# Optimization experiments

Measured on AMD Instinct MI355X. Metric: run time of the kernel, lower is better.

Reference implementation:

```python
import jax, jax.numpy as jnp
import numpy as np

N, F_IN, H1, H2, E = 100000, 256, 128, 64, 1600000


def _glorot(key, shape):
    lim = np.sqrt(6.0 / (shape[0] + shape[1]))
    return jax.random.uniform(key, shape, jnp.float32, -lim, lim)


def setup_inputs() -> dict:
    key = jax.random.key(0)
    ks = jax.random.split(key, 8)
    x = jax.random.normal(ks[0], (N, F_IN), jnp.float32)
    edge_index = jax.random.randint(ks[1], (2, E), 0, N, jnp.int64)
    return {
        "x": x,
        "w1": _glorot(ks[2], (F_IN, H1)),
        "b1": jnp.zeros((H1,), jnp.float32),
        "w2": _glorot(ks[3], (H1, H2)),
        "b2": jnp.zeros((H2,), jnp.float32),
        "w3": _glorot(ks[4], (H1, H2)),
        "b3": jnp.zeros((H2,), jnp.float32),
        "edge_index": edge_index,
    }


def _gcn_conv(x, w, b, src, dst, dinv_sqrt):
    # GCNConv: transform first, then symmetric-normalized aggregation with self-loops.
    h = x @ w                                   # [N, out]
    coef = dinv_sqrt[src] * dinv_sqrt[dst]      # [E]
    agg = jnp.zeros_like(h).at[dst].add(h[src] * coef[:, None])
    # self-loop contribution: coefficient deg^-1 per node
    agg = agg + h * (dinv_sqrt * dinv_sqrt)[:, None]
    return agg + b


def reference(x, w1, b1, w2, b2, w3, b3, edge_index):
    src, dst = edge_index[0], edge_index[1]
    n = x.shape[0]
    # degree including self-loop (edge weights all 1)
    deg = jnp.ones((n,), x.dtype).at[dst].add(1.0)
    dinv_sqrt = jax.lax.rsqrt(deg)
    hidden = jax.nn.relu(_gcn_conv(x, w1, b1, src, dst, dinv_sqrt))
    mu = _gcn_conv(hidden, w2, b2, src, dst, dinv_sqrt)
    logvar = _gcn_conv(hidden, w3, b3, src, dst, dinv_sqrt)
    return (mu, logvar)
```

## Files before the change

kernel.cpp:

```cpp
#include <hip/hip_runtime.h>


#define TPB 256
#define GSHIFT 9
#define GSIZE 512
#define PART_M 8192

typedef __attribute__((ext_vector_type(8))) short short8;
typedef __attribute__((ext_vector_type(4))) short short4v;
typedef __attribute__((ext_vector_type(4))) float floatx4;
typedef __attribute__((ext_vector_type(4))) unsigned int uint4v;

__device__ __forceinline__ void split2(float v, short& hi, short& lo) {
    unsigned u = __float_as_uint(v);
    float hf = __uint_as_float(u & 0xFFFF0000u);
    float lf = v - hf;
    hi = (short)(u >> 16);
    lo = (short)(__float_as_uint(lf) >> 16);
}

__device__ __forceinline__ short bf16_rtn(float v) {
    unsigned u = __float_as_uint(v);
    u += 0x7FFF + ((u >> 16) & 1);
    return (short)(u >> 16);
}

__device__ __forceinline__ void addrow(float* a, uint4v v) {
    a[0] += __uint_as_float(v[0] << 16); a[1] += __uint_as_float(v[0] & 0xFFFF0000u);
    a[2] += __uint_as_float(v[1] << 16); a[3] += __uint_as_float(v[1] & 0xFFFF0000u);
    a[4] += __uint_as_float(v[2] << 16); a[5] += __uint_as_float(v[2] & 0xFFFF0000u);
    a[6] += __uint_as_float(v[3] << 16); a[7] += __uint_as_float(v[3] & 0xFFFF0000u);
}

__device__ __forceinline__ void gather_accum(float* acc, const int* __restrict__ csr,
                                             int start, int deg, const uint4v* hp,
                                             int lane) {
    int j = 0;
    for (; j + 3 < deg; j += 4) {
        int s0 = csr[start + j], s1 = csr[start + j + 1];
        int s2 = csr[start + j + 2], s3 = csr[start + j + 3];
        uint4v v0 = hp[(size_t)s0 * 16 + lane];
        uint4v v1 = hp[(size_t)s1 * 16 + lane];
        uint4v v2 = hp[(size_t)s2 * 16 + lane];
        uint4v v3 = hp[(size_t)s3 * 16 + lane];
        addrow(acc, v0);
        addrow(acc, v1);
        addrow(acc, v2);
        addrow(acc, v3);
    }
    if (j + 1 < deg) {
        int s0 = csr[start + j], s1 = csr[start + j + 1];
        uint4v v0 = hp[(size_t)s0 * 16 + lane];
        uint4v v1 = hp[(size_t)s1 * 16 + lane];
        addrow(acc, v0);
        addrow(acc, v1);
        j += 2;
    }
    if (j < deg) addrow(acc, hp[(size_t)csr[start + j] * 16 + lane]);
}

__device__ __forceinline__ void gload_lds16(const void* g, void* l) {
    __builtin_amdgcn_global_load_lds(
        (const __attribute__((address_space(1))) unsigned int*)g,
        (__attribute__((address_space(3))) unsigned int*)l, 16, 0, 0);
}

__global__ __launch_bounds__(TPB) void prep_all(const float* __restrict__ w1,
                                                const float* __restrict__ w2,
                                                const float* __restrict__ b2,
                                                const float* __restrict__ w3,
                                                const float* __restrict__ b3,
                                                short* __restrict__ w1t_h,
                                                short* __restrict__ w1t_l,
                                                short* __restrict__ wct_h,
                                                short* __restrict__ wct_l,
                                                float* __restrict__ bcat,
                                                int* __restrict__ cursor) {
    int b = blockIdx.x, t0 = threadIdx.x;
    if (b < 128) {
        int t = b * TPB + t0;
        int k = t & 255, n = t >> 8;
        float v = w1[(size_t)k * 128 + n];
        short h, l;
        split2(v, h, l);
        w1t_h[t] = h;
        w1t_l[t] = l;
    } else if (b < 192) {
        int t = (b - 128) * TPB + t0;
        int k = t & 127, n = t >> 7;
        float v = (n < 64) ? w2[(size_t)k * 64 + n] : w3[(size_t)k * 64 + (n - 64)];
        short h, l;
        split2(v, h, l);
        wct_h[t] = h;
        wct_l[t] = l;
        if (t < 64) { bcat[t] = b2[t]; bcat[64 + t] = b3[t]; }
    } else {
        for (int i = t0; i < 513; i += TPB) cursor[i] = 0;
    }
}

__global__ __launch_bounds__(TPB) void group_count(const int* __restrict__ dst,
                                                   int* __restrict__ cursor, int E) {
    int* ghist = cursor;
    int* done  = cursor + 512;
    int* goff  = cursor + 513;
    __shared__ int h[256];
    __shared__ int lastFlag;
    int t = threadIdx.x;
    h[t] = 0;
    __syncthreads();
    const int4* d4 = (const int4*)dst;
    int E4 = E >> 2;
    int stride = gridDim.x * TPB;
    for (int k = blockIdx.x * TPB + t; k < E4; k += stride) {
        int4 v = d4[k];
        atomicAdd(&h[v.x >> GSHIFT], 1);
        atomicAdd(&h[v.y >> GSHIFT], 1);
        atomicAdd(&h[v.z >> GSHIFT], 1);
        atomicAdd(&h[v.w >> GSHIFT], 1);
    }
    for (int k = (E4 << 2) + blockIdx.x * TPB + t; k < E; k += stride)
        atomicAdd(&h[dst[k] >> GSHIFT], 1);
    __syncthreads();
    if (h[t]) atomicAdd(&ghist[t], h[t]);
    __threadfence();
    __syncthreads();
    if (t == 0) lastFlag = (atomicAdd(done, 1) == (int)gridDim.x - 1);
    __syncthreads();
    if (!lastFlag) return;
    int v = atomicAdd(&ghist[t], 0);
    h[t] = v;
    __syncthreads();
#pragma unroll
    for (int off = 1; off < 256; off <<= 1) {
        int x = (t >= off) ? h[t - off] : 0;
        __syncthreads();
        h[t] += x;
        __syncthreads();
    }
    goff[t] = h[t] - v;
    if (t == 255) goff[256] = h[255];
}

__global__ __launch_bounds__(256) void partition_kernel(const int* __restrict__ src,
                                                        const int* __restrict__ dst,
                                                        const int* __restrict__ goff,
                                                        int* __restrict__ gcur,
                                                        int* __restrict__ staged, int E) {
    __shared__ int sorted[PART_M];
    __shared__ int sc[256];
    __shared__ int lstart[257];
    __shared__ int cur[256];
    __shared__ int gb[256];
    int t = threadIdx.x;
    int base = blockIdx.x * PART_M;
    int mloc = min(PART_M, E - base);
    int m4 = mloc >> 2;

    sc[t] = 0;
    cur[t] = 0;
    __syncthreads();
    const int4* d4 = (const int4*)(dst + base);
    const int4* s4 = (const int4*)(src + base);
    for (int k = t; k < m4; k += 256) {
        int4 v = d4[k];
        atomicAdd(&sc[v.x >> GSHIFT], 1);
        atomicAdd(&sc[v.y >> GSHIFT], 1);
        atomicAdd(&sc[v.z >> GSHIFT], 1);
        atomicAdd(&sc[v.w >> GSHIFT], 1);
    }
    for (int k = (m4 << 2) + t; k < mloc; k += 256)
        atomicAdd(&sc[dst[base + k] >> GSHIFT], 1);
    __syncthreads();
    int v = sc[t];
    __syncthreads();
    sc[t] = v;
    __syncthreads();
#pragma unroll
    for (int off = 1; off < 256; off <<= 1) {
        int x = (t >= off) ? sc[t - off] : 0;
        __syncthreads();
        sc[t] += x;
        __syncthreads();
    }
    lstart[t] = sc[t] - v;
    if (t == 255) lstart[256] = sc[255];
    gb[t] = goff[t] + atomicAdd(&gcur[t], v);
    __syncthreads();
    for (int k = t; k < m4; k += 256) {
        int4 dv = d4[k];
        int4 sv = s4[k];
        int b0 = dv.x >> GSHIFT;
        sorted[lstart[b0] + atomicAdd(&cur[b0], 1)] = (sv.x << GSHIFT) | (dv.x & (GSIZE - 1));
        int b1 = dv.y >> GSHIFT;
        sorted[lstart[b1] + atomicAdd(&cur[b1], 1)] = (sv.y << GSHIFT) | (dv.y & (GSIZE - 1));
        int b2 = dv.z >> GSHIFT;
        sorted[lstart[b2] + atomicAdd(&cur[b2], 1)] = (sv.z << GSHIFT) | (dv.z & (GSIZE - 1));
        int b3 = dv.w >> GSHIFT;
        sorted[lstart[b3] + atomicAdd(&cur[b3], 1)] = (sv.w << GSHIFT) | (dv.w & (GSIZE - 1));
    }
    for (int k = (m4 << 2) + t; k < mloc; k += 256) {
        int d = dst[base + k];
        int s = src[base + k];
        int b = d >> GSHIFT;
        sorted[lstart[b] + atomicAdd(&cur[b], 1)] = (s << GSHIFT) | (d & (GSIZE - 1));
    }
    __syncthreads();
    for (int e = t; e < mloc; e += 256) {
        int lo = 0, hi = 256;
        while (hi - lo > 1) {
            int mid = (lo + hi) >> 1;
            if (lstart[mid] <= e) lo = mid; else hi = mid;
        }
        staged[gb[lo] + (e - lstart[lo])] = sorted[e];
    }
}

__global__ __launch_bounds__(512) void build_csr(const int* __restrict__ staged,
                                                 const int* __restrict__ goff,
                                                 int* __restrict__ cnt,
                                                 float* __restrict__ dinv,
                                                 int* __restrict__ rowptr,
                                                 int* __restrict__ csr, int N) {
    __shared__ int hist[512];
    __shared__ int sc[512];
    __shared__ int lrow[512];
    __shared__ int cur[512];
    int t = threadIdx.x;
    int g = blockIdx.x;
    int s0 = goff[g], s1 = goff[g + 1];
    hist[t] = 0;
    cur[t] = 0;
    __syncthreads();
    for (int k = s0 + t; k < s1; k += 512)
        atomicAdd(&hist[staged[k] & (GSIZE - 1)], 1);
    __syncthreads();
    int v = hist[t];
    sc[t] = v;
    __syncthreads();
#pragma unroll
    for (int off = 1; off < 512; off <<= 1) {
        int x = (t >= off) ? sc[t - off] : 0;
        __syncthreads();
        sc[t] += x;
        __syncthreads();
    }
    int rp = s0 + sc[t] - v;
    lrow[t] = rp;
    int node = (g << GSHIFT) + t;
    if (node < N) {
        rowptr[node] = rp;
        cnt[node] = v;
        dinv[node] = rsqrtf(1.0f + (float)v);
    }
    __syncthreads();
    for (int k = s0 + t; k < s1; k += 512) {
        int p = staged[k];
        int dl = p & (GSIZE - 1);
        int pos = lrow[dl] + atomicAdd(&cur[dl], 1);
        csr[pos] = p >> GSHIFT;
    }
}

__global__ __launch_bounds__(TPB) void gemm_mfma_f32in(const float* __restrict__ A,
                                                       const short* __restrict__ Bth,
                                                       const short* __restrict__ Btl,
                                                       const float* __restrict__ rs,
                                                       short* __restrict__ Cb, int M, int K) {
    __shared__ float Af[2][64 * 32];
    __shared__ short Bh[2][128 * 32];
    __shared__ short Bl[2][128 * 32];
    int t = threadIdx.x;
    int wave = t >> 6, lane = t & 63, quad = lane >> 4, l16 = lane & 15;
    int bm0 = blockIdx.x * 64;

    floatx4 acc[8];
#pragma unroll
    for (int nt = 0; nt < 8; ++nt) acc[nt] = (floatx4){0.f, 0.f, 0.f, 0.f};

    auto stage = [&](int pb, int k0) {
#pragma unroll
        for (int i = 0; i < 2; ++i) {
            int g = i * 256 + t;
            int row = g >> 3, col = g & 7;
            int gr = bm0 + row;
            if (gr >= M) gr = M - 1;
            int scol = col ^ (row & 7);
            gload_lds16(A + (size_t)gr * K + k0 + scol * 4,
                        &Af[pb][(i * 256 + wave * 64) * 4]);
        }
#pragma unroll
        for (int i = 0; i < 2; ++i) {
            int g = i * 256 + t;
            int row = g >> 2, col = g & 3;
            int scol = col ^ ((row >> 1) & 3);
            size_t off = (size_t)row * K + k0 + scol * 8;
            int lb = (i * 256 + wave * 64) * 8;
            gload_lds16(Bth + off, &Bh[pb][lb]);
            gload_lds16(Btl + off, &Bl[pb][lb]);
        }
    };

    int nk = K >> 5;
    stage(0, 0);
    __syncthreads();
    int am = wave * 16 + l16;
    int ac0 = ((quad * 2 + 0) ^ (am & 7)) * 4;
    int ac1 = ((quad * 2 + 1) ^ (am & 7)) * 4;
    int bc = (quad ^ ((l16 >> 1) & 3)) * 8;
    for (int ks = 0; ks < nk; ++ks) {
        int pb = ks & 1;
        if (ks + 1 < nk) stage(pb ^ 1, (ks + 1) << 5);
        float4 fa0 = *(const float4*)&Af[pb][am * 32 + ac0];
        float4 fa1 = *(const float4*)&Af[pb][am * 32 + ac1];
        short8 a_h, a_l;
        {
            short h, l;
            split2(fa0.x, h, l); a_h[0] = h; a_l[0] = l;
            split2(fa0.y, h, l); a_h[1] = h; a_l[1] = l;
            split2(fa0.z, h, l); a_h[2] = h; a_l[2] = l;
            split2(fa0.w, h, l); a_h[3] = h; a_l[3] = l;
            split2(fa1.x, h, l); a_h[4] = h; a_l[4] = l;
            split2(fa1.y, h, l); a_h[5] = h; a_l[5] = l;
            split2(fa1.z, h, l); a_h[6] = h; a_l[6] = l;
            split2(fa1.w, h, l); a_h[7] = h; a_l[7] = l;
        }
#pragma unroll
        for (int nt = 0; nt < 8; ++nt) {
            int bn = nt * 16 + l16;
            short8 b_h = *(const short8*)&Bh[pb][bn * 32 + bc];
            short8 b_l = *(const short8*)&Bl[pb][bn * 32 + bc];
            acc[nt] = __builtin_amdgcn_mfma_f32_16x16x32_bf16(a_l, b_h, acc[nt], 0, 0, 0);
            acc[nt] = __builtin_amdgcn_mfma_f32_16x16x32_bf16(a_h, b_l, acc[nt], 0, 0, 0);
            acc[nt] = __builtin_amdgcn_mfma_f32_16x16x32_bf16(a_h, b_h, acc[nt], 0, 0, 0);
        }
        __syncthreads();
    }
#pragma unroll
    for (int reg = 0; reg < 4; ++reg) {
        int gr = bm0 + wave * 16 + quad * 4 + reg;
        if (gr < M) {
            float s = rs[gr];
            short* cp = Cb + (size_t)gr * 128;
#pragma unroll
            for (int nt = 0; nt < 8; ++nt) cp[nt * 16 + l16] = bf16_rtn(acc[nt][reg] * s);
        }
    }
}

__global__ __launch_bounds__(TPB) void gemm_mfma_bfin(const short* __restrict__ AH,
                                                      const short* __restrict__ AL,
                                                      const short* __restrict__ Bth,
                                                      const short* __restrict__ Btl,
                                                      const float* __restrict__ rs,
                                                      short* __restrict__ Cb, int M, int K) {
    __shared__ short Ah[2][64 * 32], Al[2][64 * 32];
    __shared__ short Bh[2][128 * 32], Bl[2][128 * 32];
    int t = threadIdx.x;
    int wave = t >> 6, lane = t & 63, quad = lane >> 4, l16 = lane & 15;
    int bm0 = blockIdx.x * 64;

    floatx4 acc[8];
#pragma unroll
    for (int nt = 0; nt < 8; ++nt) acc[nt] = (floatx4){0.f, 0.f, 0.f, 0.f};

    auto stage = [&](int pb, int k0) {
        {
            int row = t >> 2, col = t & 3;
            int gr = bm0 + row;
            if (gr >= M) gr = M - 1;
            int scol = col ^ ((row >> 1) & 3);
            size_t off = (size_t)gr * K + k0 + scol * 8;
            int lb = (wave * 64) * 8;
            gload_lds16(AH + off, &Ah[pb][lb]);
            gload_lds16(AL + off, &Al[pb][lb]);
        }
#pragma unroll
        for (int i = 0; i < 2; ++i) {
            int g = i * 256 + t;
            int row = g >> 2, col = g & 3;
            int scol = col ^ ((row >> 1) & 3);
            size_t off = (size_t)row * K + k0 + scol * 8;
            int lb = (i * 256 + wave * 64) * 8;
            gload_lds16(Bth + off, &Bh[pb][lb]);
            gload_lds16(Btl + off, &Bl[pb][lb]);
        }
    };

    int nk = K >> 5;
    stage(0, 0);
    __syncthreads();
    int am = wave * 16 + l16;
    int ac = (quad ^ ((am >> 1) & 3)) * 8;
    int bc = (quad ^ ((l16 >> 1) & 3)) * 8;
    for (int ks = 0; ks < nk; ++ks) {
        int pb = ks & 1;
        if (ks + 1 < nk) stage(pb ^ 1, (ks + 1) << 5);
        short8 a_h = *(const short8*)&Ah[pb][am * 32 + ac];
        short8 a_l = *(const short8*)&Al[pb][am * 32 + ac];
#pragma unroll
        for (int nt = 0; nt < 8; ++nt) {
            int bn = nt * 16 + l16;
            short8 b_h = *(const short8*)&Bh[pb][bn * 32 + bc];
            short8 b_l = *(const short8*)&Bl[pb][bn * 32 + bc];
            acc[nt] = __builtin_amdgcn_mfma_f32_16x16x32_bf16(a_l, b_h, acc[nt], 0, 0, 0);
            acc[nt] = __builtin_amdgcn_mfma_f32_16x16x32_bf16(a_h, b_l, acc[nt], 0, 0, 0);
            acc[nt] = __builtin_amdgcn_mfma_f32_16x16x32_bf16(a_h, b_h, acc[nt], 0, 0, 0);
        }
        __syncthreads();
    }
#pragma unroll
    for (int reg = 0; reg < 4; ++reg) {
        int gr = bm0 + wave * 16 + quad * 4 + reg;
        if (gr < M) {
            float s = rs[gr];
            short* cp = Cb + (size_t)gr * 128;
#pragma unroll
            for (int nt = 0; nt < 8; ++nt) cp[nt * 16 + l16] = bf16_rtn(acc[nt][reg] * s);
        }
    }
}

__global__ __launch_bounds__(TPB) void gather_hidden(const int* __restrict__ csr,
                                                     const int* __restrict__ rowptr,
                                                     const int* __restrict__ cnt,
                                                     const float* __restrict__ dinv,
                                                     const short* __restrict__ hs,
                                                     const float* __restrict__ b1,
                                                     short* __restrict__ hidH,
                                                     short* __restrict__ hidL, int N) {
    size_t t = (size_t)blockIdx.x * TPB + threadIdx.x;
    int nid = (int)(t >> 4);
    int lane = threadIdx.x & 15;
    if (nid >= N) return;
    int start = rowptr[nid];
    int deg = cnt[nid];
    const uint4v* hp = (const uint4v*)hs;
    float acc[8] = {0, 0, 0, 0, 0, 0, 0, 0};
    addrow(acc, __builtin_nontemporal_load(&hp[(size_t)nid * 16 + lane]));
    gather_accum(acc, csr, start, deg, hp, lane);
    float di = dinv[nid];
    float4 b0 = ((const float4*)b1)[lane * 2];
    float4 b1v = ((const float4*)b1)[lane * 2 + 1];
    float bb[8] = {b0.x, b0.y, b0.z, b0.w, b1v.x, b1v.y, b1v.z, b1v.w};
    unsigned hiw[8];
    short low[8];
#pragma unroll
    for (int i = 0; i < 8; ++i) {
        float h = fmaxf(fmaf(di, acc[i], bb[i]), 0.f);
        unsigned u = __float_as_uint(h);
        hiw[i] = u >> 16;
        float hf = __uint_as_float(u & 0xFFFF0000u);
        low[i] = bf16_rtn(h - hf);
    }
    uint4v ph, pl;
    ph[0] = hiw[0] | (hiw[1] << 16);
    ph[1] = hiw[2] | (hiw[3] << 16);
    ph[2] = hiw[4] | (hiw[5] << 16);
    ph[3] = hiw[6] | (hiw[7] << 16);
    pl[0] = (unsigned short)low[0] | ((unsigned)(unsigned short)low[1] << 16);
    pl[1] = (unsigned short)low[2] | ((unsigned)(unsigned short)low[3] << 16);
    pl[2] = (unsigned short)low[4] | ((unsigned)(unsigned short)low[5] << 16);
    pl[3] = (unsigned short)low[6] | ((unsigned)(unsigned short)low[7] << 16);
    __builtin_nontemporal_store(ph, &((uint4v*)hidH)[(size_t)nid * 16 + lane]);
    __builtin_nontemporal_store(pl, &((uint4v*)hidL)[(size_t)nid * 16 + lane]);
}

__global__ __launch_bounds__(TPB) void gather_out(const int* __restrict__ csr,
                                                  const int* __restrict__ rowptr,
                                                  const int* __restrict__ cnt,
                                                  const float* __restrict__ dinv,
                                                  const short* __restrict__ hs,
                                                  const float* __restrict__ bcat,
                                                  float* __restrict__ out, int N) {
    size_t t = (size_t)blockIdx.x * TPB + threadIdx.x;
    int nid = (int)(t >> 4);
    int lane = threadIdx.x & 15;
    if (nid >= N) return;
    int start = rowptr[nid];
    int deg = cnt[nid];
    const uint4v* hp = (const uint4v*)hs;
    float acc[8] = {0, 0, 0, 0, 0, 0, 0, 0};
    addrow(acc, __builtin_nontemporal_load(&hp[(size_t)nid * 16 + lane]));
    gather_accum(acc, csr, start, deg, hp, lane);
    float di = dinv[nid];
    float4 b0 = ((const float4*)bcat)[lane * 2];
    float4 b1v = ((const float4*)bcat)[lane * 2 + 1];
    floatx4 r0, r1;
    r0[0] = fmaf(di, acc[0], b0.x);
    r0[1] = fmaf(di, acc[1], b0.y);
    r0[2] = fmaf(di, acc[2], b0.z);
    r0[3] = fmaf(di, acc[3], b0.w);
    r1[0] = fmaf(di, acc[4], b1v.x);
    r1[1] = fmaf(di, acc[5], b1v.y);
    r1[2] = fmaf(di, acc[6], b1v.z);
    r1[3] = fmaf(di, acc[7], b1v.w);
    int f = lane * 8;
    float* dp = (f < 64) ? (out + (size_t)nid * 64 + f)
                         : (out + (size_t)N * 64 + (size_t)nid * 64 + (f - 64));
    __builtin_nontemporal_store(r0, (floatx4*)dp);
    __builtin_nontemporal_store(r1, (floatx4*)(dp + 4));
}

extern "C" void kernel_launch(void* const* d_in, const int* in_sizes, int n_in,
                              void* d_out, int out_size, void* d_ws, size_t ws_size,
                              hipStream_t stream) {
    const float* x  = (const float*)d_in[0];
    const float* w1 = (const float*)d_in[1];
    const float* b1 = (const float*)d_in[2];
    const float* w2 = (const float*)d_in[3];
    const float* b2 = (const float*)d_in[4];
    const float* w3 = (const float*)d_in[5];
    const float* b3 = (const float*)d_in[6];
    const int*   ei = (const int*)d_in[7];

    const int N = in_sizes[0] / 256;
    const int E = in_sizes[7] / 2;
    const int K1 = 256;

    float* out = (float*)d_out;

    size_t nh = (size_t)N * 128;
    short* hs1    = (short*)d_ws;
    short* hidH   = hs1 + nh;
    short* hidL   = hidH + nh;
    short* hs2    = hidL + nh;
    int*   cnt    = (int*)(hs2 + nh);
    float* dinv   = (float*)(cnt + N);
    int*   rowptr = (int*)(dinv + N);
    int*   cursor = rowptr + N;
    int*   bsum   = cursor + N;
    float* bcat   = (float*)(bsum + 512);
    short* w1t_h  = (short*)(bcat + 128);
    short* w1t_l  = w1t_h + 128 * 256;
    short* wct_h  = w1t_l + 128 * 256;
    short* wct_l  = wct_h + 128 * 128;
    int*   csr    = (int*)(wct_l + 128 * 128);

    const int* srcp = ei;
    const int* dstp = ei + E;

    const int ngrp = (N + GSIZE - 1) >> GSHIFT;
    int* gcur   = cursor + 256;
    int* goff   = cursor + 513;
    int* staged = (int*)hs2;

    prep_all<<<193, TPB, 0, stream>>>(w1, w2, b2, w3, b3, w1t_h, w1t_l, wct_h, wct_l,
                                      bcat, cursor);

    int gc_blocks = ((E >> 2) + TPB * 4 - 1) / (TPB * 4);
    group_count<<<gc_blocks, TPB, 0, stream>>>(dstp, cursor, E);
    partition_kernel<<<(E + PART_M - 1) / PART_M, 256, 0, stream>>>(srcp, dstp, goff, gcur,
                                                                    staged, E);
    build_csr<<<ngrp, 512, 0, stream>>>(staged, goff, cnt, dinv, rowptr, csr, N);

    gemm_mfma_f32in<<<(N + 63) / 64, TPB, 0, stream>>>(x, w1t_h, w1t_l, dinv, hs1, N, K1);

    size_t gthreads = (size_t)N * 16;
    gather_hidden<<<(unsigned)((gthreads + TPB - 1) / TPB), TPB, 0, stream>>>(
        csr, rowptr, cnt, dinv, hs1, b1, hidH, hidL, N);

    gemm_mfma_bfin<<<(N + 63) / 64, TPB, 0, stream>>>(hidH, hidL, wct_h, wct_l, dinv, hs2, N, 128);

    gather_out<<<(unsigned)((gthreads + TPB - 1) / TPB), TPB, 0, stream>>>(
        csr, rowptr, cnt, dinv, hs2, bcat, out, N);
}
```

Before: 425.7 us.

## Scatter partitioned edges directly to global and cooperatively load CSR indices

The partition kernel drops its shared-memory local sort, the prefix scan and the binary-search copy-out. It now writes each edge straight to its global bucket slot using per-block atomic cursors, and the block size is halved so more blocks run. The gather loop loads 16 neighbour indices at once across the 16-lane group and broadcasts them with shuffles, which removes the redundant per-lane index loads. The direct scatter writes to global memory are less coalesced than before.

```diff
diff --git a/kernel.cpp b/kernel.cpp
--- a/kernel.cpp
+++ b/kernel.cpp
@@ -4,7 +4,7 @@
 #define TPB 256
 #define GSHIFT 9
 #define GSIZE 512
-#define PART_M 8192
+#define PART_M 4096
 
 typedef __attribute__((ext_vector_type(8))) short short8;
 typedef __attribute__((ext_vector_type(4))) short short4v;
@@ -34,29 +34,32 @@
 
 __device__ __forceinline__ void gather_accum(float* acc, const int* __restrict__ csr,
                                              int start, int deg, const uint4v* hp,
-                                             int lane) {
-    int j = 0;
-    for (; j + 3 < deg; j += 4) {
-        int s0 = csr[start + j], s1 = csr[start + j + 1];
-        int s2 = csr[start + j + 2], s3 = csr[start + j + 3];
-        uint4v v0 = hp[(size_t)s0 * 16 + lane];
-        uint4v v1 = hp[(size_t)s1 * 16 + lane];
-        uint4v v2 = hp[(size_t)s2 * 16 + lane];
-        uint4v v3 = hp[(size_t)s3 * 16 + lane];
-        addrow(acc, v0);
-        addrow(acc, v1);
-        addrow(acc, v2);
-        addrow(acc, v3);
-    }
-    if (j + 1 < deg) {
-        int s0 = csr[start + j], s1 = csr[start + j + 1];
-        uint4v v0 = hp[(size_t)s0 * 16 + lane];
-        uint4v v1 = hp[(size_t)s1 * 16 + lane];
-        addrow(acc, v0);
-        addrow(acc, v1);
-        j += 2;
-    }
-    if (j < deg) addrow(acc, hp[(size_t)csr[start + j] * 16 + lane]);
+                                             int l16) {
+    for (int jj = 0; jj < deg; jj += 16) {
+        int rem = deg - jj;
+        if (rem > 16) rem = 16;
+        int il = (l16 < rem) ? l16 : rem - 1;
+        int myIdx = csr[start + jj + il];
+        int r = 0;
+        for (; r + 3 < rem; r += 4) {
+            int i0 = __shfl(myIdx, r + 0, 16);
+            int i1 = __shfl(myIdx, r + 1, 16);
+            int i2 = __shfl(myIdx, r + 2, 16);
+            int i3 = __shfl(myIdx, r + 3, 16);
+            uint4v v0 = hp[(size_t)i0 * 16 + l16];
+            uint4v v1 = hp[(size_t)i1 * 16 + l16];
+            uint4v v2 = hp[(size_t)i2 * 16 + l16];
+            uint4v v3 = hp[(size_t)i3 * 16 + l16];
+            addrow(acc, v0);
+            addrow(acc, v1);
+            addrow(acc, v2);
+            addrow(acc, v3);
+        }
+        for (; r < rem; ++r) {
+            int i = __shfl(myIdx, r, 16);
+            addrow(acc, hp[(size_t)i * 16 + l16]);
+        }
+    }
 }
 
 __device__ __forceinline__ void gload_lds16(const void* g, void* l) {
@@ -147,9 +150,7 @@
                                                         const int* __restrict__ goff,
                                                         int* __restrict__ gcur,
                                                         int* __restrict__ staged, int E) {
-    __shared__ int sorted[PART_M];
     __shared__ int sc[256];
-    __shared__ int lstart[257];
     __shared__ int cur[256];
     __shared__ int gb[256];
     int t = threadIdx.x;
@@ -173,46 +174,25 @@
         atomicAdd(&sc[dst[base + k] >> GSHIFT], 1);
     __syncthreads();
     int v = sc[t];
-    __syncthreads();
-    sc[t] = v;
-    __syncthreads();
-#pragma unroll
-    for (int off = 1; off < 256; off <<= 1) {
-        int x = (t >= off) ? sc[t - off] : 0;
-        __syncthreads();
-        sc[t] += x;
-        __syncthreads();
-    }
-    lstart[t] = sc[t] - v;
-    if (t == 255) lstart[256] = sc[255];
-    gb[t] = goff[t] + atomicAdd(&gcur[t], v);
+    gb[t] = v ? goff[t] + atomicAdd(&gcur[t], v) : 0;
     __syncthreads();
     for (int k = t; k < m4; k += 256) {
         int4 dv = d4[k];
         int4 sv = s4[k];
         int b0 = dv.x >> GSHIFT;
-        sorted[lstart[b0] + atomicAdd(&cur[b0], 1)] = (sv.x << GSHIFT) | (dv.x & (GSIZE - 1));
+        staged[gb[b0] + atomicAdd(&cur[b0], 1)] = (sv.x << GSHIFT) | (dv.x & (GSIZE - 1));
         int b1 = dv.y >> GSHIFT;
-        sorted[lstart[b1] + atomicAdd(&cur[b1], 1)] = (sv.y << GSHIFT) | (dv.y & (GSIZE - 1));
+        staged[gb[b1] + atomicAdd(&cur[b1], 1)] = (sv.y << GSHIFT) | (dv.y & (GSIZE - 1));
         int b2 = dv.z >> GSHIFT;
-        sorted[lstart[b2] + atomicAdd(&cur[b2], 1)] = (sv.z << GSHIFT) | (dv.z & (GSIZE - 1));
+        staged[gb[b2] + atomicAdd(&cur[b2], 1)] = (sv.z << GSHIFT) | (dv.z & (GSIZE - 1));
         int b3 = dv.w >> GSHIFT;
-        sorted[lstart[b3] + atomicAdd(&cur[b3], 1)] = (sv.w << GSHIFT) | (dv.w & (GSIZE - 1));
+        staged[gb[b3] + atomicAdd(&cur[b3], 1)] = (sv.w << GSHIFT) | (dv.w & (GSIZE - 1));
     }
     for (int k = (m4 << 2) + t; k < mloc; k += 256) {
         int d = dst[base + k];
         int s = src[base + k];
         int b = d >> GSHIFT;
-        sorted[lstart[b] + atomicAdd(&cur[b], 1)] = (s << GSHIFT) | (d & (GSIZE - 1));
-    }
-    __syncthreads();
-    for (int e = t; e < mloc; e += 256) {
-        int lo = 0, hi = 256;
-        while (hi - lo > 1) {
-            int mid = (lo + hi) >> 1;
-            if (lstart[mid] <= e) lo = mid; else hi = mid;
-        }
-        staged[gb[lo] + (e - lstart[lo])] = sorted[e];
+        staged[gb[b] + atomicAdd(&cur[b], 1)] = (s << GSHIFT) | (d & (GSIZE - 1));
     }
 }
 
```

New measurement: 412.7 us. 1.03x faster.
